# Kernel optimization log

Measured on AMD Instinct MI355X. Metric: run time of the kernel, lower is better.

The kernel has to match this reference:

```python
import jax, jax.numpy as jnp
import numpy as np

N_NODES = 100000
N_EDGES = 1600000
D_IN = 128
D_OUT = 128
DROP_P = 0.5


def setup_inputs() -> dict:
    key = jax.random.key(0)
    k1, k2, k3, k4, k5, k6 = jax.random.split(key, 6)
    x = jax.random.normal(k1, (N_NODES, D_IN), dtype=jnp.float32)
    # xavier_normal init for w
    std = (2.0 / (D_IN + D_OUT)) ** 0.5
    w = jax.random.normal(k2, (D_IN, D_OUT), dtype=jnp.float32) * std
    b = jax.random.normal(k3, (D_OUT,), dtype=jnp.float32) * 0.01
    edge_row = jax.random.randint(k4, (N_EDGES,), 0, N_NODES, dtype=jnp.int32)
    edge_col = jax.random.randint(k5, (N_EDGES,), 0, N_NODES, dtype=jnp.int32)
    # normalized adjacency weights (e.g. 1/sqrt(d_i d_j)); use uniform positives
    edge_val = jax.random.uniform(k6, (N_EDGES,), dtype=jnp.float32)
    # dropout mask: keep with prob (1-p), scaled by 1/(1-p)
    km = jax.random.fold_in(key, 7)
    keep = jax.random.uniform(km, (N_NODES, D_IN)) >= DROP_P
    dropout_mask = keep.astype(jnp.float32) / (1.0 - DROP_P)
    return {"x": x, "w": w, "b": b, "edge_row": edge_row,
            "edge_col": edge_col, "edge_val": edge_val,
            "dropout_mask": dropout_mask}


def reference(x, w, b, edge_row, edge_col, edge_val, dropout_mask):
    # dropout (training mode) -> dense mm -> spmm(adj, xw) -> +b -> relu
    h = (x * dropout_mask) @ w                      # [N, D_OUT]
    msgs = h[edge_col] * edge_val[:, None]          # gather src feats, scale [E, D_OUT]
    agg = jax.ops.segment_sum(msgs, edge_row, num_segments=N_NODES)  # scatter-add to dst
    return jax.nn.relu(agg + b)
```

## Files before the change

### kernel.cpp

```cpp
#include <hip/hip_runtime.h>

#define N_NODES 100000
#define N_EDGES 1600000
#define D 128
#define MAXDEG 48

#define GEMM_NB ((N_NODES + 63) / 64)
#define HIST_NB (N_EDGES / 256)
#define TOTAL_NB (GEMM_NB + HIST_NB)

typedef __attribute__((ext_vector_type(8))) short short8;
typedef __attribute__((ext_vector_type(4))) short short4v;
typedef __attribute__((ext_vector_type(4))) float floatx4;
typedef __attribute__((ext_vector_type(2))) float floatx2;

__device__ __forceinline__ short f2bf(float f) {
    unsigned u = __float_as_uint(f);
    u += 0x7FFFu + ((u >> 16) & 1u);
    return (short)(u >> 16);
}

#define LDSK 136
__global__ __launch_bounds__(256) void gemm_hist_fill(const float* __restrict__ x,
                                                      const float* __restrict__ mask,
                                                      const float* __restrict__ w,
                                                      unsigned short* __restrict__ h,
                                                      const int* __restrict__ erow,
                                                      const int* __restrict__ ecol,
                                                      const float* __restrict__ eval,
                                                      int* __restrict__ deg,
                                                      unsigned long long* __restrict__ pairs) {
    const unsigned bid = blockIdx.x;
    const int t = threadIdx.x;

    if (bid % 5 != 0) {
        const int hi = (int)(bid - bid / 5 - 1);
        const int e = hi * 256 + t;
        const int r = erow[e];
        const int k = atomicAdd(&deg[r], 1);
        if (k < MAXDEG) {
            const unsigned long long pv =
                (unsigned long long)(unsigned)ecol[e] |
                ((unsigned long long)(unsigned)__float_as_uint(eval[e]) << 32);
            pairs[(size_t)r * MAXDEG + k] = pv;
        }
        return;
    }
    const int gb = (int)(bid / 5);

    const int wave = t >> 6, lane = t & 63;
    const int m = lane & 15, quad = lane >> 4;
    const int r0w = gb * 64 + wave * 16;
    int arow = r0w + m;
    if (arow >= N_NODES) arow = N_NODES - 1;
    const floatx4* xp4 = (const floatx4*)(x + (size_t)arow * D);
    const floatx4* mp4 = (const floatx4*)(mask + (size_t)arow * D);

    floatx4 xv[8], mv[8];
#pragma unroll
    for (int kc = 0; kc < 4; ++kc) {
        xv[2 * kc]     = __builtin_nontemporal_load(xp4 + kc * 8 + quad * 2);
        xv[2 * kc + 1] = __builtin_nontemporal_load(xp4 + kc * 8 + quad * 2 + 1);
        mv[2 * kc]     = __builtin_nontemporal_load(mp4 + kc * 8 + quad * 2);
        mv[2 * kc + 1] = __builtin_nontemporal_load(mp4 + kc * 8 + quad * 2 + 1);
    }

    __shared__ short w_s[128 * LDSK];
#pragma unroll
    for (int i = 0; i < 4; ++i) {
        const int id = t + 256 * i;
        const int n0 = (id & 31) * 4;
        const int k0 = (id >> 5) * 4;
        short tr[4][4];
#pragma unroll
        for (int r = 0; r < 4; ++r) {
            const float4 wv = *(const float4*)(w + (size_t)(k0 + r) * D + n0);
            tr[r][0] = f2bf(wv.x); tr[r][1] = f2bf(wv.y);
            tr[r][2] = f2bf(wv.z); tr[r][3] = f2bf(wv.w);
        }
#pragma unroll
        for (int c = 0; c < 4; ++c) {
            short4v v = {tr[0][c], tr[1][c], tr[2][c], tr[3][c]};
            *(short4v*)(&w_s[(n0 + c) * LDSK + k0]) = v;
        }
    }
    __syncthreads();

    floatx4 acc[8];
#pragma unroll
    for (int tt = 0; tt < 8; ++tt) acc[tt] = (floatx4){0.f, 0.f, 0.f, 0.f};

#pragma unroll
    for (int kc = 0; kc < 4; ++kc) {
        const int kb = kc * 32 + quad * 8;
        const floatx4 xa = xv[2 * kc];
        const floatx4 xb = xv[2 * kc + 1];
        const floatx4 ma = mv[2 * kc];
        const floatx4 mb = mv[2 * kc + 1];
        short8 a;
#pragma unroll
        for (int j = 0; j < 4; ++j) a[j] = f2bf(xa[j] * ma[j]);
#pragma unroll
        for (int j = 0; j < 4; ++j) a[4 + j] = f2bf(xb[j] * mb[j]);
#pragma unroll
        for (int tt = 0; tt < 8; ++tt) {
            const short8 bfrag = *(const short8*)(&w_s[(tt * 16 + m) * LDSK + kb]);
            acc[tt] = __builtin_amdgcn_mfma_f32_16x16x32_bf16(a, bfrag, acc[tt], 0, 0, 0);
        }
    }

    __syncthreads();
    short* ep = w_s + wave * 16 * LDSK;
#pragma unroll
    for (int tt = 0; tt < 8; ++tt) {
        const int col = tt * 16 + m;
#pragma unroll
        for (int i = 0; i < 4; ++i)
            ep[(quad * 4 + i) * LDSK + col] = f2bf(acc[tt][i]);
    }
    __syncthreads();

    const int rrow = lane >> 2;
    const int chunk = lane & 3;
    const int gr = r0w + rrow;
    if (gr < N_NODES) {
        const short* src = ep + rrow * LDSK + chunk * 32;
        unsigned short* dst = h + (size_t)gr * D + chunk * 32;
#pragma unroll
        for (int j = 0; j < 4; ++j)
            *(short8*)(dst + j * 8) = *(const short8*)(src + j * 8);
    }
}

__global__ __launch_bounds__(256) void gather_kernel(const unsigned* __restrict__ h2,
                                                     const int* __restrict__ deg,
                                                     const unsigned long long* __restrict__ pairs,
                                                     const float* __restrict__ b,
                                                     float* __restrict__ out) {
    const int lane = threadIdx.x & 63;
    const int rA = blockIdx.x * 8 + (threadIdx.x >> 6) * 2;
    const int rB = rA + 1;

    int dgA = deg[rA]; if (dgA > MAXDEG) dgA = MAXDEG;
    int dgB = deg[rB]; if (dgB > MAXDEG) dgB = MAXDEG;

    const int pl = (lane < MAXDEG) ? lane : (MAXDEG - 1);
    const unsigned long long pvA = pairs[(size_t)rA * MAXDEG + pl];
    const unsigned long long pvB = pairs[(size_t)rB * MAXDEG + pl];
    const unsigned cAv = (unsigned)pvA;
    const unsigned wAv = (unsigned)(pvA >> 32);
    const unsigned cBv = (unsigned)pvB;
    const unsigned wBv = (unsigned)(pvB >> 32);

    float axA = 0.f, ayA = 0.f, axB = 0.f, ayB = 0.f;
    const int mx = (dgA > dgB) ? dgA : dgB;

    for (int b0 = 0; b0 < mx; b0 += 16) {
        unsigned uA[16], uB[16];
#pragma unroll
        for (int jj = 0; jj < 16; ++jj) {
            const int j = b0 + jj;
            const unsigned colA = (j < dgA)
                ? (unsigned)__builtin_amdgcn_readlane((int)cAv, j) : 0u;
            uA[jj] = h2[(size_t)colA * 64 + lane];
            const unsigned colB = (j < dgB)
                ? (unsigned)__builtin_amdgcn_readlane((int)cBv, j) : 0u;
            uB[jj] = h2[(size_t)colB * 64 + lane];
        }
#pragma unroll
        for (int jj = 0; jj < 16; ++jj) {
            const int j = b0 + jj;
            const float vA = (j < dgA)
                ? __uint_as_float((unsigned)__builtin_amdgcn_readlane((int)wAv, j)) : 0.f;
            const float vB = (j < dgB)
                ? __uint_as_float((unsigned)__builtin_amdgcn_readlane((int)wBv, j)) : 0.f;
            axA += __uint_as_float(uA[jj] << 16) * vA;
            ayA += __uint_as_float(uA[jj] & 0xFFFF0000u) * vA;
            axB += __uint_as_float(uB[jj] << 16) * vB;
            ayB += __uint_as_float(uB[jj] & 0xFFFF0000u) * vB;
        }
    }

    const float2 bv = ((const float2*)b)[lane];
    floatx2 oA, oB;
    oA.x = fmaxf(axA + bv.x, 0.f);
    oA.y = fmaxf(ayA + bv.y, 0.f);
    oB.x = fmaxf(axB + bv.x, 0.f);
    oB.y = fmaxf(ayB + bv.y, 0.f);
    __builtin_nontemporal_store(oA, (floatx2*)(out + (size_t)rA * D) + lane);
    __builtin_nontemporal_store(oB, (floatx2*)(out + (size_t)rB * D) + lane);
}

extern "C" void kernel_launch(void* const* d_in, const int* in_sizes, int n_in,
                              void* d_out, int out_size, void* d_ws, size_t ws_size,
                              hipStream_t stream) {
    const float* x    = (const float*)d_in[0];
    const float* w    = (const float*)d_in[1];
    const float* b    = (const float*)d_in[2];
    const int*   erow = (const int*)d_in[3];
    const int*   ecol = (const int*)d_in[4];
    const float* eval = (const float*)d_in[5];
    const float* mask = (const float*)d_in[6];
    float* out = (float*)d_out;

    char* base = (char*)d_ws;
    unsigned short* h = (unsigned short*)(base);
    int* deg          = (int*)(base + 25600000);
    unsigned long long* pairs = (unsigned long long*)(base + 26000000);

    (void)hipMemsetAsync(deg, 0, N_NODES * sizeof(int), stream);

    gemm_hist_fill<<<TOTAL_NB, 256, 0, stream>>>(x, mask, w, h, erow, ecol, eval, deg, pairs);
    gather_kernel<<<N_NODES / 8, 256, 0, stream>>>((const unsigned*)h, deg, pairs, b, out);
}
```

Before: 289.2 us.

## Fuse GEMM/histogram and gather into one persistent cooperative kernel with grid sync

Merges the two kernels into a single persistent cooperative kernel of 1024 blocks. Each block grid-strides over the GEMM and histogram-fill work, then hits a grid-wide sync, then grid-strides over the gather. The aim is to remove the second launch and the inter-kernel gap. In exchange it limits parallelism to 1024 resident blocks, adds grid-sync cost and an extra __syncthreads per GEMM tile, and falls back to the old two-kernel path if the cooperative launch fails.

```diff
diff --git a/kernel.cpp b/kernel.cpp
--- a/kernel.cpp
+++ b/kernel.cpp
@@ -1,4 +1,7 @@
 #include <hip/hip_runtime.h>
+#include <hip/hip_cooperative_groups.h>
+
+namespace cg = cooperative_groups;
 
 #define N_NODES 100000
 #define N_EDGES 1600000
@@ -8,6 +11,8 @@
 #define GEMM_NB ((N_NODES + 63) / 64)
 #define HIST_NB (N_EDGES / 256)
 #define TOTAL_NB (GEMM_NB + HIST_NB)
+#define GATHER_NB (N_NODES / 8)
+#define COOP_NB 1024
 
 typedef __attribute__((ext_vector_type(8))) short short8;
 typedef __attribute__((ext_vector_type(4))) short short4v;
@@ -21,6 +26,182 @@
 }
 
 #define LDSK 136
+
+__global__ __launch_bounds__(256, 4) void fused_all(const float* __restrict__ x,
+                                                    const float* __restrict__ mask,
+                                                    const float* __restrict__ w,
+                                                    unsigned short* __restrict__ h,
+                                                    const int* __restrict__ erow,
+                                                    const int* __restrict__ ecol,
+                                                    const float* __restrict__ eval,
+                                                    int* __restrict__ deg,
+                                                    unsigned long long* __restrict__ pairs,
+                                                    const float* __restrict__ b,
+                                                    float* __restrict__ out) {
+    const int t = threadIdx.x;
+    const int wave = t >> 6, lane = t & 63;
+    __shared__ short w_s[128 * LDSK];
+
+    for (unsigned vb = blockIdx.x; vb < TOTAL_NB; vb += COOP_NB) {
+        if (vb % 5 != 0) {
+            const int hi = (int)(vb - vb / 5 - 1);
+            const int e = hi * 256 + t;
+            const int r = erow[e];
+            const int k = atomicAdd(&deg[r], 1);
+            if (k < MAXDEG) {
+                const unsigned long long pv =
+                    (unsigned long long)(unsigned)ecol[e] |
+                    ((unsigned long long)(unsigned)__float_as_uint(eval[e]) << 32);
+                pairs[(size_t)r * MAXDEG + k] = pv;
+            }
+            continue;
+        }
+        const int gb = (int)(vb / 5);
+
+        const int m = lane & 15, quad = lane >> 4;
+        const int r0w = gb * 64 + wave * 16;
+        int arow = r0w + m;
+        if (arow >= N_NODES) arow = N_NODES - 1;
+        const floatx4* xp4 = (const floatx4*)(x + (size_t)arow * D);
+        const floatx4* mp4 = (const floatx4*)(mask + (size_t)arow * D);
+
+        floatx4 xv[8], mv[8];
+#pragma unroll
+        for (int kc = 0; kc < 4; ++kc) {
+            xv[2 * kc]     = __builtin_nontemporal_load(xp4 + kc * 8 + quad * 2);
+            xv[2 * kc + 1] = __builtin_nontemporal_load(xp4 + kc * 8 + quad * 2 + 1);
+            mv[2 * kc]     = __builtin_nontemporal_load(mp4 + kc * 8 + quad * 2);
+            mv[2 * kc + 1] = __builtin_nontemporal_load(mp4 + kc * 8 + quad * 2 + 1);
+        }
+
+#pragma unroll
+        for (int i = 0; i < 4; ++i) {
+            const int id = t + 256 * i;
+            const int n0 = (id & 31) * 4;
+            const int k0 = (id >> 5) * 4;
+            short tr[4][4];
+#pragma unroll
+            for (int r = 0; r < 4; ++r) {
+                const float4 wv = *(const float4*)(w + (size_t)(k0 + r) * D + n0);
+                tr[r][0] = f2bf(wv.x); tr[r][1] = f2bf(wv.y);
+                tr[r][2] = f2bf(wv.z); tr[r][3] = f2bf(wv.w);
+            }
+#pragma unroll
+            for (int c = 0; c < 4; ++c) {
+                short4v v = {tr[0][c], tr[1][c], tr[2][c], tr[3][c]};
+                *(short4v*)(&w_s[(n0 + c) * LDSK + k0]) = v;
+            }
+        }
+        __syncthreads();
+
+        floatx4 acc[8];
+#pragma unroll
+        for (int tt = 0; tt < 8; ++tt) acc[tt] = (floatx4){0.f, 0.f, 0.f, 0.f};
+
+#pragma unroll
+        for (int kc = 0; kc < 4; ++kc) {
+            const int kb = kc * 32 + quad * 8;
+            const floatx4 xa = xv[2 * kc];
+            const floatx4 xb = xv[2 * kc + 1];
+            const floatx4 ma = mv[2 * kc];
+            const floatx4 mb = mv[2 * kc + 1];
+            short8 a;
+#pragma unroll
+            for (int j = 0; j < 4; ++j) a[j] = f2bf(xa[j] * ma[j]);
+#pragma unroll
+            for (int j = 0; j < 4; ++j) a[4 + j] = f2bf(xb[j] * mb[j]);
+#pragma unroll
+            for (int tt = 0; tt < 8; ++tt) {
+                const short8 bfrag = *(const short8*)(&w_s[(tt * 16 + m) * LDSK + kb]);
+                acc[tt] = __builtin_amdgcn_mfma_f32_16x16x32_bf16(a, bfrag, acc[tt], 0, 0, 0);
+            }
+        }
+
+        __syncthreads();
+        short* ep = w_s + wave * 16 * LDSK;
+#pragma unroll
+        for (int tt = 0; tt < 8; ++tt) {
+            const int col = tt * 16 + m;
+#pragma unroll
+            for (int i = 0; i < 4; ++i)
+                ep[(quad * 4 + i) * LDSK + col] = f2bf(acc[tt][i]);
+        }
+        __syncthreads();
+
+        const int rrow = lane >> 2;
+        const int chunk = lane & 3;
+        const int gr = r0w + rrow;
+        if (gr < N_NODES) {
+            const short* src = ep + rrow * LDSK + chunk * 32;
+            unsigned short* dst = h + (size_t)gr * D + chunk * 32;
+#pragma unroll
+            for (int j = 0; j < 4; ++j)
+                *(short8*)(dst + j * 8) = *(const short8*)(src + j * 8);
+        }
+        __syncthreads();
+    }
+
+    __threadfence();
+    cg::this_grid().sync();
+    __threadfence();
+
+    const unsigned* __restrict__ h2 = (const unsigned*)h;
+    const float2 bv = ((const float2*)b)[lane];
+
+    for (unsigned vb = blockIdx.x; vb < GATHER_NB; vb += COOP_NB) {
+        const int rA = (int)vb * 8 + wave * 2;
+        const int rB = rA + 1;
+
+        int dgA = deg[rA]; if (dgA > MAXDEG) dgA = MAXDEG;
+        int dgB = deg[rB]; if (dgB > MAXDEG) dgB = MAXDEG;
+
+        const int pl = (lane < MAXDEG) ? lane : (MAXDEG - 1);
+        const unsigned long long pvA = pairs[(size_t)rA * MAXDEG + pl];
+        const unsigned long long pvB = pairs[(size_t)rB * MAXDEG + pl];
+        const unsigned cAv = (unsigned)pvA;
+        const unsigned wAv = (unsigned)(pvA >> 32);
+        const unsigned cBv = (unsigned)pvB;
+        const unsigned wBv = (unsigned)(pvB >> 32);
+
+        float axA = 0.f, ayA = 0.f, axB = 0.f, ayB = 0.f;
+        const int mx = (dgA > dgB) ? dgA : dgB;
+
+        for (int b0 = 0; b0 < mx; b0 += 16) {
+            unsigned uA[16], uB[16];
+#pragma unroll
+            for (int jj = 0; jj < 16; ++jj) {
+                const int j = b0 + jj;
+                const unsigned colA = (j < dgA)
+                    ? (unsigned)__builtin_amdgcn_readlane((int)cAv, j) : 0u;
+                uA[jj] = h2[(size_t)colA * 64 + lane];
+                const unsigned colB = (j < dgB)
+                    ? (unsigned)__builtin_amdgcn_readlane((int)cBv, j) : 0u;
+                uB[jj] = h2[(size_t)colB * 64 + lane];
+            }
+#pragma unroll
+            for (int jj = 0; jj < 16; ++jj) {
+                const int j = b0 + jj;
+                const float vA = (j < dgA)
+                    ? __uint_as_float((unsigned)__builtin_amdgcn_readlane((int)wAv, j)) : 0.f;
+                const float vB = (j < dgB)
+                    ? __uint_as_float((unsigned)__builtin_amdgcn_readlane((int)wBv, j)) : 0.f;
+                axA += __uint_as_float(uA[jj] << 16) * vA;
+                ayA += __uint_as_float(uA[jj] & 0xFFFF0000u) * vA;
+                axB += __uint_as_float(uB[jj] << 16) * vB;
+                ayB += __uint_as_float(uB[jj] & 0xFFFF0000u) * vB;
+            }
+        }
+
+        floatx2 oA, oB;
+        oA.x = fmaxf(axA + bv.x, 0.f);
+        oA.y = fmaxf(ayA + bv.y, 0.f);
+        oB.x = fmaxf(axB + bv.x, 0.f);
+        oB.y = fmaxf(ayB + bv.y, 0.f);
+        __builtin_nontemporal_store(oA, (floatx2*)(out + (size_t)rA * D) + lane);
+        __builtin_nontemporal_store(oB, (floatx2*)(out + (size_t)rB * D) + lane);
+    }
+}
+
 __global__ __launch_bounds__(256) void gemm_hist_fill(const float* __restrict__ x,
                                                       const float* __restrict__ mask,
                                                       const float* __restrict__ w,
@@ -210,6 +391,17 @@
 
     (void)hipMemsetAsync(deg, 0, N_NODES * sizeof(int), stream);
 
-    gemm_hist_fill<<<TOTAL_NB, 256, 0, stream>>>(x, mask, w, h, erow, ecol, eval, deg, pairs);
-    gather_kernel<<<N_NODES / 8, 256, 0, stream>>>((const unsigned*)h, deg, pairs, b, out);
+    void* kargs[] = {(void*)&x, (void*)&mask, (void*)&w, (void*)&h,
+                     (void*)&erow, (void*)&ecol, (void*)&eval,
+                     (void*)&deg, (void*)&pairs, (void*)&b, (void*)&out};
+    hipError_t rc = hipLaunchCooperativeKernel((const void*)fused_all,
+                                               dim3(COOP_NB), dim3(256),
+                                               kargs, 0, stream);
+    if (rc != hipSuccess) {
+        (void)hipGetLastError();
+        gemm_hist_fill<<<TOTAL_NB, 256, 0, stream>>>(x, mask, w, h, erow, ecol,
+                                                     eval, deg, pairs);
+        gather_kernel<<<N_NODES / 8, 256, 0, stream>>>((const unsigned*)h, deg,
+                                                       pairs, b, out);
+    }
 }
```

Result: slower. 658.1 us (+127.6%).

## Bucket edges by 32-row groups and sort per bucket in LDS before gathering

Applied to the files above, without the earlier changes.

Edges are binned into buckets of 32 destination rows instead of per-row slots. Each bucket counter is padded to its own 64-byte line, the local row index is packed into the upper bits of the column field, and records go into a 768-entry buffer per bucket. The gather kernel loads one bucket into shared memory, counting-sorts it by row, then runs the same readlane gather per row pair. This removes the hard per-row degree cap of 48 and cuts contention on 100k scattered row counters and the cost of scattered pair writes. In exchange it adds an LDS sort pass and imposes a per-bucket capacity limit.

```diff
diff --git a/kernel.cpp b/kernel.cpp
--- a/kernel.cpp
+++ b/kernel.cpp
@@ -3,7 +3,10 @@
 #define N_NODES 100000
 #define N_EDGES 1600000
 #define D 128
-#define MAXDEG 48
+
+#define BROWS 32
+#define NBKT 3125
+#define CAP 768
 
 #define GEMM_NB ((N_NODES + 63) / 64)
 #define HIST_NB (N_EDGES / 256)
@@ -28,8 +31,8 @@
                                                       const int* __restrict__ erow,
                                                       const int* __restrict__ ecol,
                                                       const float* __restrict__ eval,
-                                                      int* __restrict__ deg,
-                                                      unsigned long long* __restrict__ pairs) {
+                                                      int* __restrict__ cnt,
+                                                      unsigned long long* __restrict__ ebuf) {
     const unsigned bid = blockIdx.x;
     const int t = threadIdx.x;
 
@@ -37,12 +40,13 @@
         const int hi = (int)(bid - bid / 5 - 1);
         const int e = hi * 256 + t;
         const int r = erow[e];
-        const int k = atomicAdd(&deg[r], 1);
-        if (k < MAXDEG) {
+        const int bkt = r >> 5;
+        const int k = atomicAdd(&cnt[bkt * 16], 1);
+        if (k < CAP) {
             const unsigned long long pv =
-                (unsigned long long)(unsigned)ecol[e] |
+                (unsigned long long)((unsigned)ecol[e] | ((unsigned)(r & 31) << 20)) |
                 ((unsigned long long)(unsigned)__float_as_uint(eval[e]) << 32);
-            pairs[(size_t)r * MAXDEG + k] = pv;
+            ebuf[(size_t)bkt * CAP + k] = pv;
         }
         return;
     }
@@ -132,63 +136,103 @@
     }
 }
 
-__global__ __launch_bounds__(256) void gather_kernel(const unsigned* __restrict__ h2,
-                                                     const int* __restrict__ deg,
-                                                     const unsigned long long* __restrict__ pairs,
-                                                     const float* __restrict__ b,
-                                                     float* __restrict__ out) {
-    const int lane = threadIdx.x & 63;
-    const int rA = blockIdx.x * 8 + (threadIdx.x >> 6) * 2;
-    const int rB = rA + 1;
-
-    int dgA = deg[rA]; if (dgA > MAXDEG) dgA = MAXDEG;
-    int dgB = deg[rB]; if (dgB > MAXDEG) dgB = MAXDEG;
-
-    const int pl = (lane < MAXDEG) ? lane : (MAXDEG - 1);
-    const unsigned long long pvA = pairs[(size_t)rA * MAXDEG + pl];
-    const unsigned long long pvB = pairs[(size_t)rB * MAXDEG + pl];
-    const unsigned cAv = (unsigned)pvA;
-    const unsigned wAv = (unsigned)(pvA >> 32);
-    const unsigned cBv = (unsigned)pvB;
-    const unsigned wBv = (unsigned)(pvB >> 32);
-
-    float axA = 0.f, ayA = 0.f, axB = 0.f, ayB = 0.f;
-    const int mx = (dgA > dgB) ? dgA : dgB;
-
-    for (int b0 = 0; b0 < mx; b0 += 16) {
-        unsigned uA[16], uB[16];
-#pragma unroll
-        for (int jj = 0; jj < 16; ++jj) {
-            const int j = b0 + jj;
-            const unsigned colA = (j < dgA)
-                ? (unsigned)__builtin_amdgcn_readlane((int)cAv, j) : 0u;
-            uA[jj] = h2[(size_t)colA * 64 + lane];
-            const unsigned colB = (j < dgB)
-                ? (unsigned)__builtin_amdgcn_readlane((int)cBv, j) : 0u;
-            uB[jj] = h2[(size_t)colB * 64 + lane];
-        }
-#pragma unroll
-        for (int jj = 0; jj < 16; ++jj) {
-            const int j = b0 + jj;
-            const float vA = (j < dgA)
-                ? __uint_as_float((unsigned)__builtin_amdgcn_readlane((int)wAv, j)) : 0.f;
-            const float vB = (j < dgB)
-                ? __uint_as_float((unsigned)__builtin_amdgcn_readlane((int)wBv, j)) : 0.f;
-            axA += __uint_as_float(uA[jj] << 16) * vA;
-            ayA += __uint_as_float(uA[jj] & 0xFFFF0000u) * vA;
-            axB += __uint_as_float(uB[jj] << 16) * vB;
-            ayB += __uint_as_float(uB[jj] & 0xFFFF0000u) * vB;
-        }
-    }
+__global__ __launch_bounds__(256, 4) void bucket_gather(const unsigned* __restrict__ h2,
+                                                        const int* __restrict__ cnt,
+                                                        const unsigned long long* __restrict__ ebuf,
+                                                        const float* __restrict__ b,
+                                                        float* __restrict__ out) {
+    __shared__ unsigned long long recRaw[CAP];
+    __shared__ unsigned long long recSrt[CAP];
+    __shared__ int cnt32[BROWS];
+    __shared__ int offs[BROWS];
+    __shared__ int fill[BROWS];
+    const int t = threadIdx.x;
+    const int bkt = blockIdx.x;
+    const int wave = t >> 6, lane = t & 63;
+
+    if (t < BROWS) { cnt32[t] = 0; fill[t] = 0; }
+    __syncthreads();
+
+    int n = cnt[bkt * 16]; if (n > CAP) n = CAP;
+    const unsigned long long* eb = ebuf + (size_t)bkt * CAP;
+    for (int i = t; i < n; i += 256) {
+        const unsigned long long rec = eb[i];
+        recRaw[i] = rec;
+        atomicAdd(&cnt32[((unsigned)rec >> 20) & 31u], 1);
+    }
+    for (int i = n + t; i < CAP; i += 256) recSrt[i] = 0ull;
+    __syncthreads();
+
+    if (t == 0) {
+        int s = 0;
+#pragma unroll
+        for (int r = 0; r < BROWS; ++r) { offs[r] = s; s += cnt32[r]; }
+    }
+    __syncthreads();
+
+    for (int i = t; i < n; i += 256) {
+        const unsigned long long rec = recRaw[i];
+        const int row = (int)(((unsigned)rec >> 20) & 31u);
+        const int pos = offs[row] + atomicAdd(&fill[row], 1);
+        recSrt[pos] = rec;
+    }
+    __syncthreads();
 
     const float2 bv = ((const float2*)b)[lane];
-    floatx2 oA, oB;
-    oA.x = fmaxf(axA + bv.x, 0.f);
-    oA.y = fmaxf(ayA + bv.y, 0.f);
-    oB.x = fmaxf(axB + bv.x, 0.f);
-    oB.y = fmaxf(ayB + bv.y, 0.f);
-    __builtin_nontemporal_store(oA, (floatx2*)(out + (size_t)rA * D) + lane);
-    __builtin_nontemporal_store(oB, (floatx2*)(out + (size_t)rB * D) + lane);
+    const int r0 = bkt * BROWS;
+
+    for (int pr = wave; pr < 16; pr += 4) {
+        const int rA = pr * 2, rB = rA + 1;
+        const int dgA = cnt32[rA];
+        const int dgB = cnt32[rB];
+        const int pA = offs[rA], pB = offs[rB];
+
+        const int plA = (lane < dgA) ? lane : (dgA > 0 ? dgA - 1 : 0);
+        const int plB = (lane < dgB) ? lane : (dgB > 0 ? dgB - 1 : 0);
+        const unsigned long long pvA = recSrt[pA + plA];
+        const unsigned long long pvB = recSrt[pB + plB];
+        const unsigned cAv = (unsigned)pvA;
+        const unsigned wAv = (unsigned)(pvA >> 32);
+        const unsigned cBv = (unsigned)pvB;
+        const unsigned wBv = (unsigned)(pvB >> 32);
+
+        float axA = 0.f, ayA = 0.f, axB = 0.f, ayB = 0.f;
+        const int mx = (dgA > dgB) ? dgA : dgB;
+
+        for (int b0 = 0; b0 < mx; b0 += 16) {
+            unsigned uA[16], uB[16];
+#pragma unroll
+            for (int jj = 0; jj < 16; ++jj) {
+                const int j = b0 + jj;
+                const unsigned colA = (j < dgA)
+                    ? ((unsigned)__builtin_amdgcn_readlane((int)cAv, j) & 0xFFFFFu) : 0u;
+                uA[jj] = h2[(size_t)colA * 64 + lane];
+                const unsigned colB = (j < dgB)
+                    ? ((unsigned)__builtin_amdgcn_readlane((int)cBv, j) & 0xFFFFFu) : 0u;
+                uB[jj] = h2[(size_t)colB * 64 + lane];
+            }
+#pragma unroll
+            for (int jj = 0; jj < 16; ++jj) {
+                const int j = b0 + jj;
+                const float vA = (j < dgA)
+                    ? __uint_as_float((unsigned)__builtin_amdgcn_readlane((int)wAv, j)) : 0.f;
+                const float vB = (j < dgB)
+                    ? __uint_as_float((unsigned)__builtin_amdgcn_readlane((int)wBv, j)) : 0.f;
+                axA += __uint_as_float(uA[jj] << 16) * vA;
+                ayA += __uint_as_float(uA[jj] & 0xFFFF0000u) * vA;
+                axB += __uint_as_float(uB[jj] << 16) * vB;
+                ayB += __uint_as_float(uB[jj] & 0xFFFF0000u) * vB;
+            }
+        }
+
+        floatx2 oA, oB;
+        oA.x = fmaxf(axA + bv.x, 0.f);
+        oA.y = fmaxf(ayA + bv.y, 0.f);
+        oB.x = fmaxf(axB + bv.x, 0.f);
+        oB.y = fmaxf(ayB + bv.y, 0.f);
+        __builtin_nontemporal_store(oA, (floatx2*)(out + (size_t)(r0 + rA) * D) + lane);
+        __builtin_nontemporal_store(oB, (floatx2*)(out + (size_t)(r0 + rB) * D) + lane);
+    }
 }
 
 extern "C" void kernel_launch(void* const* d_in, const int* in_sizes, int n_in,
@@ -205,11 +249,11 @@
 
     char* base = (char*)d_ws;
     unsigned short* h = (unsigned short*)(base);
-    int* deg          = (int*)(base + 25600000);
-    unsigned long long* pairs = (unsigned long long*)(base + 26000000);
-
-    (void)hipMemsetAsync(deg, 0, N_NODES * sizeof(int), stream);
-
-    gemm_hist_fill<<<TOTAL_NB, 256, 0, stream>>>(x, mask, w, h, erow, ecol, eval, deg, pairs);
-    gather_kernel<<<N_NODES / 8, 256, 0, stream>>>((const unsigned*)h, deg, pairs, b, out);
-}
+    int* cnt          = (int*)(base + 25600000);
+    unsigned long long* ebuf = (unsigned long long*)(base + 25800000);
+
+    (void)hipMemsetAsync(cnt, 0, NBKT * 16 * sizeof(int), stream);
+
+    gemm_hist_fill<<<TOTAL_NB, 256, 0, stream>>>(x, mask, w, h, erow, ecol, eval, cnt, ebuf);
+    bucket_gather<<<NBKT, 256, 0, stream>>>((const unsigned*)h, cnt, ebuf, b, out);
+}
```

Measured after the change: 291.1 us. Within noise of the previous version (+0.6%).
